# Optimization experiments

Measured on AMD Instinct MI355X. Metric: run time of the kernel, lower is better.

The kernel has to match this reference:

```python
import jax, jax.numpy as jnp
import numpy as np

NHEAD = 8
HEAD_DIM = 32  # per-head dim d; C = NHEAD * HEAD_DIM = 256
NEG_INF = -1e9


def setup_inputs() -> dict:
    key = jax.random.key(0)
    k1, k2, k3, k4, k5 = jax.random.split(key, 5)
    B, L, C = 8, 1024, NHEAD * HEAD_DIM
    query = jax.random.normal(k1, (B, L, C), dtype=jnp.float32)
    key_t = jax.random.normal(k2, (B, L, C), dtype=jnp.float32)
    value = jax.random.normal(k3, (B, L, C), dtype=jnp.float32)
    hard_mask = jax.random.randint(k4, (B, L), 0, 2).astype(bool)
    bias = jax.random.normal(k5, (B, L, L), dtype=jnp.float32)
    return {"query": query, "key": key_t, "value": value,
            "hard_mask": hard_mask, "bias": bias}


def reference(query, key, value, hard_mask, bias):
    # Faithful to the hard-mask path: attention is computed only among
    # active tokens (hard_mask True); inactive positions pass `value` through.
    # Masking inactive KEYS with -inf in the softmax is mathematically
    # identical to the sort/gather/slice/SDPA/scatter-unsort in the original.
    B, L, C = query.shape
    H, D = NHEAD, HEAD_DIM
    scale = 1.0 / jnp.sqrt(jnp.asarray(D, query.dtype))

    def split_heads(t):  # (B, L, C) -> (B, H, L, D)
        return t.reshape(B, L, H, D).transpose(0, 2, 1, 3)

    q, k, v = split_heads(query), split_heads(key), split_heads(value)

    # scores: (B, H, Lq, Lk); bias broadcasts over heads
    scores = jnp.einsum('bhld,bhmd->bhlm', q, k) * scale + bias[:, None, :, :]
    scores = jnp.where(hard_mask[:, None, None, :], scores, NEG_INF)
    attn = jax.nn.softmax(scores, axis=-1)
    out = jnp.einsum('bhlm,bhmd->bhld', attn, v)          # (B, H, L, D)
    out = out.transpose(0, 2, 1, 3).reshape(B, L, C)      # (B, L, C)

    # inactive query positions return the raw value (scatter-back behavior)
    out = jnp.where(hard_mask[:, :, None], out, value)

    # torch.stack over per-item (1, L, C) results -> (B, 1, L, C)
    return out[:, None, :, :]
```

## Files before the change

kernel.cpp:

```cpp
#include <hip/hip_runtime.h>
#include <hip/hip_bf16.h>

#define B_    8
#define H_    8
#define L_    1024
#define D_    32
#define C_    256
#define NK    64
#define PSTR  72

typedef __attribute__((ext_vector_type(8))) short bf16x8;
typedef __attribute__((ext_vector_type(4))) float f32x4;

__device__ inline unsigned short f2bf(float f) {
    union { float f; unsigned int u; } x; x.f = f;
    return (unsigned short)((x.u + 0x7fffu + ((x.u >> 16) & 1u)) >> 16);
}

__device__ inline unsigned int pk_bf16(float lo, float hi) {
    union { __hip_bfloat162 h; unsigned int u; } c;
    c.h = __float22bfloat162_rn(make_float2(lo, hi));
    return c.u;
}

__global__ __launch_bounds__(256) void prep_all(
    const float* __restrict__ k, const float* __restrict__ v,
    const float* __restrict__ bias, const int* __restrict__ mask,
    unsigned short* __restrict__ kfrag, unsigned short* __restrict__ vfrag,
    unsigned short* __restrict__ bfragT)
{
    const int tid = threadIdx.x;
    const int blk = blockIdx.x;
    __shared__ float sKf[64 * 36];
    __shared__ float sVf[64 * 33];
    __shared__ float sMadd[L_];

    if (blk < 1024) {
        const int bh = blk >> 4, c = blk & 15;
        const int b = bh >> 3, h = bh & 7;
        {
            const int row = tid >> 2, seg = tid & 3;
            const size_t src = (size_t)(b * L_ + c * 64 + row) * C_ + h * D_ + seg * 8;
            float4 a = *(const float4*)(k + src);
            float4 d = *(const float4*)(k + src + 4);
            *(float4*)(sKf + row * 36 + seg * 8) = a;
            *(float4*)(sKf + row * 36 + seg * 8 + 4) = d;
            float4 va = *(const float4*)(v + src);
            float4 vd = *(const float4*)(v + src + 4);
            float* vr = sVf + row * 33 + seg * 8;
            vr[0] = va.x; vr[1] = va.y; vr[2] = va.z; vr[3] = va.w;
            vr[4] = vd.x; vr[5] = vd.y; vr[6] = vd.z; vr[7] = vd.w;
        }
        __syncthreads();
        const int ln = tid & 63, u = tid >> 6;
        const int l16 = ln & 15, quad = ln >> 4;
        {
            const float* src = sKf + (u * 16 + l16) * 36 + quad * 8;
            float4 a = *(const float4*)src;
            float4 d = *(const float4*)(src + 4);
            uint4 o = { pk_bf16(a.x, a.y), pk_bf16(a.z, a.w),
                        pk_bf16(d.x, d.y), pk_bf16(d.z, d.w) };
            *(uint4*)(kfrag + (size_t)blk * 2048 + u * 512 + ln * 8) = o;
        }
        {
            const int s2 = u >> 1, nt = u & 1;
            float vals[8];
#pragma unroll
            for (int j = 0; j < 8; ++j)
                vals[j] = sVf[(s2 * 32 + quad * 8 + j) * 33 + nt * 16 + l16];
            uint4 o = { pk_bf16(vals[0], vals[1]), pk_bf16(vals[2], vals[3]),
                        pk_bf16(vals[4], vals[5]), pk_bf16(vals[6], vals[7]) };
            *(uint4*)(vfrag + (size_t)blk * 2048 + s2 * 1024 + nt * 512 + ln * 8) = o;
        }
    } else {
        const int bblk = blk - 1024;
        const int b = bblk >> 6, strip = bblk & 63;
        {
            int4 m = ((const int4*)(mask + b * L_))[tid];
            sMadd[tid * 4 + 0] = m.x ? 0.f : -1e9f;
            sMadd[tid * 4 + 1] = m.y ? 0.f : -1e9f;
            sMadd[tid * 4 + 2] = m.z ? 0.f : -1e9f;
            sMadd[tid * 4 + 3] = m.w ? 0.f : -1e9f;
        }
        __syncthreads();
        const int l16 = tid >> 4, ntp = (tid >> 2) & 3, qp = tid & 3;
        const float* brow = bias + ((size_t)(b * L_) + strip * 16 + l16) * L_;
        unsigned short* obase = bfragT + (size_t)bblk * 16384
                                + (qp * 16 + l16) * 16 + ntp * 4;
        const int koff = ntp * 16 + qp * 4;
#pragma unroll 4
        for (int c = 0; c < 16; ++c) {
            const int key = c * 64 + koff;
            float4 a = *(const float4*)(brow + key);
            const float* mp = sMadd + key;
            uint2 o = { pk_bf16(a.x + mp[0], a.y + mp[1]),
                        pk_bf16(a.z + mp[2], a.w + mp[3]) };
            *(uint2*)(obase + c * 1024) = o;
        }
    }
}

__global__ __launch_bounds__(256, 4) void attn_fa3(
    const float* __restrict__ q,
    const float* __restrict__ v,
    const int*   __restrict__ mask,
    const unsigned short* __restrict__ kfrag,
    const unsigned short* __restrict__ vfrag,
    const unsigned short* __restrict__ bfragT,
    float*       __restrict__ out)
{
    __shared__ __align__(16) unsigned short sP[4][16 * PSTR];

    const int tid  = threadIdx.x;
    const int wv   = tid >> 6;
    const int ln   = tid & 63;
    const int l16  = ln & 15;
    const int quad = ln >> 4;

    const int blk = blockIdx.x;
    const int h   = blk >> 7;
    const int rem = blk & 127;
    const int b   = rem >> 4;
    const int qt  = rem & 15;
    const int strip = qt * 4 + wv;
    const int q0  = strip * 16;
    const int bh  = b * H_ + h;

    const float scale = 0.17677669529663687f;

    bf16x8 qfrag;
    {
        const float* qp = q + ((size_t)(b * L_ + q0 + l16) * C_ + h * D_ + quad * 8);
        float4 a = ((const float4*)qp)[0];
        float4 c = ((const float4*)qp)[1];
        __align__(16) unsigned int u[4] = {
            pk_bf16(a.x * scale, a.y * scale), pk_bf16(a.z * scale, a.w * scale),
            pk_bf16(c.x * scale, c.y * scale), pk_bf16(c.z * scale, c.w * scale)};
        qfrag = *(const bf16x8*)u;
    }

    bf16x8 onesf;
#pragma unroll
    for (int i = 0; i < 8; ++i) onesf[i] = (short)0x3F80;

    const unsigned short* kf_base = kfrag  + (size_t)bh * 32768 + ln * 8;
    const unsigned short* vf_base = vfrag  + (size_t)bh * 32768 + ln * 8;
    const unsigned short* bm_base = bfragT + (size_t)(b * 64 + strip) * 16384 + ln * 16;
    unsigned short* const sPw = &sP[wv][0];

    f32x4 Oacc[2] = {{0.f,0.f,0.f,0.f},{0.f,0.f,0.f,0.f}};
    f32x4 Lacc    = {0.f,0.f,0.f,0.f};

    bf16x8 kf[4];
    uint4  bm[2];
#pragma unroll
    for (int nt = 0; nt < 4; ++nt)
        kf[nt] = *(const bf16x8*)(kf_base + nt * 512);
    bm[0] = *(const uint4*)(bm_base);
    bm[1] = *(const uint4*)(bm_base + 8);

    for (int c = 0; c < 16; ++c) {
        bf16x8 vf[4];
#pragma unroll
        for (int u2 = 0; u2 < 4; ++u2)
            vf[u2] = *(const bf16x8*)(vf_base + c * 2048 + u2 * 512);

        f32x4 S[4];
#pragma unroll
        for (int nt = 0; nt < 4; ++nt)
            S[nt] = __builtin_amdgcn_mfma_f32_16x16x32_bf16(
                kf[nt], qfrag, (f32x4){0.f,0.f,0.f,0.f}, 0, 0, 0);

        const int cn = (c < 15) ? c + 1 : 15;
        bf16x8 kfN[4];
        uint4  bmN[2];
#pragma unroll
        for (int nt = 0; nt < 4; ++nt)
            kfN[nt] = *(const bf16x8*)(kf_base + cn * 2048 + nt * 512);
        bmN[0] = *(const uint4*)(bm_base + cn * 1024);
        bmN[1] = *(const uint4*)(bm_base + cn * 1024 + 8);

        unsigned short* const prow = sPw + l16 * PSTR + quad * 4;
#pragma unroll
        for (int nt = 0; nt < 4; ++nt) {
            const unsigned int w0 = ((const unsigned int*)bm)[2 * nt];
            const unsigned int w1 = ((const unsigned int*)bm)[2 * nt + 1];
            const float b0 = __uint_as_float(w0 << 16);
            const float b1 = __uint_as_float(w0 & 0xffff0000u);
            const float b2 = __uint_as_float(w1 << 16);
            const float b3 = __uint_as_float(w1 & 0xffff0000u);
            const float p0 = __expf(S[nt][0] + b0);
            const float p1 = __expf(S[nt][1] + b1);
            const float p2 = __expf(S[nt][2] + b2);
            const float p3 = __expf(S[nt][3] + b3);
            uint2 pw = { pk_bf16(p0, p1), pk_bf16(p2, p3) };
            *(uint2*)(prow + nt * 16) = pw;
        }

#pragma unroll
        for (int s2 = 0; s2 < 2; ++s2) {
            bf16x8 pf = *(const bf16x8*)(sPw + l16 * PSTR + s2 * 32 + quad * 8);
            Lacc = __builtin_amdgcn_mfma_f32_16x16x32_bf16(pf, onesf, Lacc, 0, 0, 0);
            Oacc[0] = __builtin_amdgcn_mfma_f32_16x16x32_bf16(pf, vf[s2 * 2 + 0], Oacc[0], 0, 0, 0);
            Oacc[1] = __builtin_amdgcn_mfma_f32_16x16x32_bf16(pf, vf[s2 * 2 + 1], Oacc[1], 0, 0, 0);
        }

#pragma unroll
        for (int nt = 0; nt < 4; ++nt) kf[nt] = kfN[nt];
        bm[0] = bmN[0];
        bm[1] = bmN[1];
    }

#pragma unroll
    for (int r = 0; r < 4; ++r) {
        const int qrow = q0 + quad * 4 + r;
        const int active = mask[b * L_ + qrow];
        const float inv = 1.f / Lacc[r];
        const size_t base = (size_t)(b * L_ + qrow) * C_ + h * D_;
#pragma unroll
        for (int nt = 0; nt < 2; ++nt) {
            const size_t idx = base + nt * 16 + l16;
            out[idx] = active ? Oacc[nt][r] * inv : v[idx];
        }
    }
}

#define MQ    64
#define KSTR  48
#define VSTR  72

__global__ __launch_bounds__(256) void masked_attn_mfma(
    const float* __restrict__ q,
    const float* __restrict__ k,
    const float* __restrict__ v,
    const int*   __restrict__ mask,
    const float* __restrict__ bias,
    float*       __restrict__ out)
{
    __shared__ __align__(16) unsigned short sQ[MQ][KSTR];
    __shared__ __align__(16) unsigned short sKt[NK][KSTR];
    __shared__ __align__(16) unsigned short sVt[D_][VSTR];
    __shared__ __align__(16) unsigned short sP2[4][16][VSTR];
    __shared__ float sMadd2[NK];

    const int tid  = threadIdx.x;
    const int wv   = tid >> 6;
    const int ln   = tid & 63;
    const int l16  = ln & 15;
    const int quad = ln >> 4;

    const int blk = blockIdx.x;
    const int h   = blk & 7;
    const int qt  = (blk >> 3) & 15;
    const int b   = blk >> 7;
    const int q0  = qt * MQ;
    const float scale = 0.17677669529663687f;

    {
        const int row = tid >> 2, d0 = (tid & 3) * 8;
        const float* src = q + ((size_t)(b * L_ + q0 + row) * C_ + h * D_ + d0);
        float4 a = ((const float4*)src)[0];
        float4 c = ((const float4*)src)[1];
        __align__(16) unsigned short t8[8] = {
            f2bf(a.x), f2bf(a.y), f2bf(a.z), f2bf(a.w),
            f2bf(c.x), f2bf(c.y), f2bf(c.z), f2bf(c.w)};
        *(int4*)&sQ[row][d0] = *(const int4*)t8;
    }
    __syncthreads();

    const bf16x8 qfrag = *(const bf16x8*)&sQ[wv * 16 + l16][quad * 8];
    f32x4 Oacc[2] = {{0.f,0.f,0.f,0.f},{0.f,0.f,0.f,0.f}};
    float lsum[4] = {0.f, 0.f, 0.f, 0.f};

    for (int j0 = 0; j0 < L_; j0 += NK) {
        __syncthreads();
        {
            const int row = tid >> 2, d0 = (tid & 3) * 8;
            const size_t src = (size_t)(b * L_ + j0 + row) * C_ + h * D_ + d0;
            float4 ka = ((const float4*)(k + src))[0];
            float4 kb = ((const float4*)(k + src))[1];
            __align__(16) unsigned short t8[8] = {
                f2bf(ka.x), f2bf(ka.y), f2bf(ka.z), f2bf(ka.w),
                f2bf(kb.x), f2bf(kb.y), f2bf(kb.z), f2bf(kb.w)};
            *(int4*)&sKt[row][d0] = *(const int4*)t8;

            float4 va = ((const float4*)(v + src))[0];
            float4 vb = ((const float4*)(v + src))[1];
            sVt[d0 + 0][row] = f2bf(va.x);
            sVt[d0 + 1][row] = f2bf(va.y);
            sVt[d0 + 2][row] = f2bf(va.z);
            sVt[d0 + 3][row] = f2bf(va.w);
            sVt[d0 + 4][row] = f2bf(vb.x);
            sVt[d0 + 5][row] = f2bf(vb.y);
            sVt[d0 + 6][row] = f2bf(vb.z);
            sVt[d0 + 7][row] = f2bf(vb.w);
            if (tid < NK) sMadd2[tid] = mask[b * L_ + j0 + tid] ? 0.f : -1e9f;
        }
        __syncthreads();

        bf16x8 kf[4];
#pragma unroll
        for (int nt = 0; nt < 4; ++nt)
            kf[nt] = *(const bf16x8*)&sKt[nt * 16 + l16][quad * 8];

        f32x4 S[4];
#pragma unroll
        for (int nt = 0; nt < 4; ++nt)
            S[nt] = __builtin_amdgcn_mfma_f32_16x16x32_bf16(
                qfrag, kf[nt], (f32x4){0.f,0.f,0.f,0.f}, 0, 0, 0);

        float psum[4] = {0.f, 0.f, 0.f, 0.f};
        const size_t brow0 = (size_t)(b * L_ + q0 + wv * 16 + quad * 4) * L_ + j0;
#pragma unroll
        for (int nt = 0; nt < 4; ++nt) {
            const float madd = sMadd2[nt * 16 + l16];
#pragma unroll
            for (int r = 0; r < 4; ++r) {
                float s = S[nt][r] * scale + bias[brow0 + (size_t)r * L_ + nt * 16 + l16] + madd;
                float p = __expf(s);
                psum[r] += p;
                S[nt][r] = p;
            }
        }
#pragma unroll
        for (int nt = 0; nt < 4; ++nt)
#pragma unroll
            for (int r = 0; r < 4; ++r)
                sP2[wv][quad * 4 + r][nt * 16 + l16] = f2bf(S[nt][r]);
#pragma unroll
        for (int r = 0; r < 4; ++r) {
            float t = psum[r];
            t += __shfl_xor(t, 1);
            t += __shfl_xor(t, 2);
            t += __shfl_xor(t, 4);
            t += __shfl_xor(t, 8);
            lsum[r] += t;
        }
#pragma unroll
        for (int s2 = 0; s2 < 2; ++s2) {
            bf16x8 pf = *(const bf16x8*)&sP2[wv][l16][s2 * 32 + quad * 8];
#pragma unroll
            for (int nt = 0; nt < 2; ++nt) {
                bf16x8 vf = *(const bf16x8*)&sVt[nt * 16 + l16][s2 * 32 + quad * 8];
                Oacc[nt] = __builtin_amdgcn_mfma_f32_16x16x32_bf16(pf, vf, Oacc[nt], 0, 0, 0);
            }
        }
    }
#pragma unroll
    for (int r = 0; r < 4; ++r) {
        const int qg = q0 + wv * 16 + quad * 4 + r;
        const int active = mask[b * L_ + qg];
        const size_t obase = (size_t)(b * L_ + qg) * C_ + h * D_;
        const float inv = 1.f / lsum[r];
#pragma unroll
        for (int nt = 0; nt < 2; ++nt) {
            float val;
            if (active) val = Oacc[nt][r] * inv;
            else        val = v[obase + nt * 16 + l16];
            out[obase + nt * 16 + l16] = val;
        }
    }
}

extern "C" void kernel_launch(void* const* d_in, const int* in_sizes, int n_in,
                              void* d_out, int out_size, void* d_ws, size_t ws_size,
                              hipStream_t stream) {
    const float* q    = (const float*)d_in[0];
    const float* k    = (const float*)d_in[1];
    const float* v    = (const float*)d_in[2];
    const int*   mask = (const int*)d_in[3];
    const float* bias = (const float*)d_in[4];
    float* out = (float*)d_out;

    if (ws_size >= (size_t)24 * 1024 * 1024) {
        unsigned short* kfrag  = (unsigned short*)d_ws;
        unsigned short* vfrag  = kfrag + (size_t)2 * 1024 * 1024;
        unsigned short* bfragT = vfrag + (size_t)2 * 1024 * 1024;
        prep_all<<<1536, 256, 0, stream>>>(k, v, bias, mask, kfrag, vfrag, bfragT);
        attn_fa3<<<1024, 256, 0, stream>>>(q, v, mask, kfrag, vfrag, bfragT, out);
    } else {
        masked_attn_mfma<<<1024, 256, 0, stream>>>(q, k, v, mask, bias, out);
    }
}
```

Measured before the change: 130.5 us.

## Process two query strips per wave to reuse K/V fragments

```diff
diff --git a/kernel.cpp b/kernel.cpp
--- a/kernel.cpp
+++ b/kernel.cpp
@@ -100,7 +100,7 @@
     }
 }
 
-__global__ __launch_bounds__(256, 4) void attn_fa3(
+__global__ __launch_bounds__(128, 2) void attn_fa5(
     const float* __restrict__ q,
     const float* __restrict__ v,
     const int*   __restrict__ mask,
@@ -109,7 +109,7 @@
     const unsigned short* __restrict__ bfragT,
     float*       __restrict__ out)
 {
-    __shared__ __align__(16) unsigned short sP[4][16 * PSTR];
+    __shared__ __align__(16) unsigned short sP[2][32 * PSTR];
 
     const int tid  = threadIdx.x;
     const int wv   = tid >> 6;
@@ -122,21 +122,22 @@
     const int rem = blk & 127;
     const int b   = rem >> 4;
     const int qt  = rem & 15;
-    const int strip = qt * 4 + wv;
-    const int q0  = strip * 16;
+    const int q0  = qt * 64 + wv * 32;
+    const int strip0 = q0 >> 4;
     const int bh  = b * H_ + h;
 
     const float scale = 0.17677669529663687f;
 
-    bf16x8 qfrag;
-    {
-        const float* qp = q + ((size_t)(b * L_ + q0 + l16) * C_ + h * D_ + quad * 8);
+    bf16x8 qfrag[2];
+#pragma unroll
+    for (int st = 0; st < 2; ++st) {
+        const float* qp = q + ((size_t)(b * L_ + q0 + st * 16 + l16) * C_ + h * D_ + quad * 8);
         float4 a = ((const float4*)qp)[0];
         float4 c = ((const float4*)qp)[1];
         __align__(16) unsigned int u[4] = {
             pk_bf16(a.x * scale, a.y * scale), pk_bf16(a.z * scale, a.w * scale),
             pk_bf16(c.x * scale, c.y * scale), pk_bf16(c.z * scale, c.w * scale)};
-        qfrag = *(const bf16x8*)u;
+        qfrag[st] = *(const bf16x8*)u;
     }
 
     bf16x8 onesf;
@@ -145,19 +146,25 @@
 
     const unsigned short* kf_base = kfrag  + (size_t)bh * 32768 + ln * 8;
     const unsigned short* vf_base = vfrag  + (size_t)bh * 32768 + ln * 8;
-    const unsigned short* bm_base = bfragT + (size_t)(b * 64 + strip) * 16384 + ln * 16;
+    const unsigned short* bm_base[2] = {
+        bfragT + (size_t)(b * 64 + strip0    ) * 16384 + ln * 16,
+        bfragT + (size_t)(b * 64 + strip0 + 1) * 16384 + ln * 16 };
     unsigned short* const sPw = &sP[wv][0];
 
-    f32x4 Oacc[2] = {{0.f,0.f,0.f,0.f},{0.f,0.f,0.f,0.f}};
-    f32x4 Lacc    = {0.f,0.f,0.f,0.f};
+    f32x4 Oacc[2][2] = {{{0.f,0.f,0.f,0.f},{0.f,0.f,0.f,0.f}},
+                        {{0.f,0.f,0.f,0.f},{0.f,0.f,0.f,0.f}}};
+    f32x4 Lacc[2]    = {{0.f,0.f,0.f,0.f},{0.f,0.f,0.f,0.f}};
 
     bf16x8 kf[4];
-    uint4  bm[2];
+    uint4  bm[2][2];
 #pragma unroll
     for (int nt = 0; nt < 4; ++nt)
         kf[nt] = *(const bf16x8*)(kf_base + nt * 512);
-    bm[0] = *(const uint4*)(bm_base);
-    bm[1] = *(const uint4*)(bm_base + 8);
+#pragma unroll
+    for (int st = 0; st < 2; ++st) {
+        bm[st][0] = *(const uint4*)(bm_base[st]);
+        bm[st][1] = *(const uint4*)(bm_base[st] + 8);
+    }
 
     for (int c = 0; c < 16; ++c) {
         bf16x8 vf[4];
@@ -165,62 +172,80 @@
         for (int u2 = 0; u2 < 4; ++u2)
             vf[u2] = *(const bf16x8*)(vf_base + c * 2048 + u2 * 512);
 
-        f32x4 S[4];
-#pragma unroll
-        for (int nt = 0; nt < 4; ++nt)
-            S[nt] = __builtin_amdgcn_mfma_f32_16x16x32_bf16(
-                kf[nt], qfrag, (f32x4){0.f,0.f,0.f,0.f}, 0, 0, 0);
+        f32x4 S[2][4];
+#pragma unroll
+        for (int st = 0; st < 2; ++st)
+#pragma unroll
+            for (int nt = 0; nt < 4; ++nt)
+                S[st][nt] = __builtin_amdgcn_mfma_f32_16x16x32_bf16(
+                    kf[nt], qfrag[st], (f32x4){0.f,0.f,0.f,0.f}, 0, 0, 0);
 
         const int cn = (c < 15) ? c + 1 : 15;
         bf16x8 kfN[4];
-        uint4  bmN[2];
+        uint4  bmN[2][2];
 #pragma unroll
         for (int nt = 0; nt < 4; ++nt)
             kfN[nt] = *(const bf16x8*)(kf_base + cn * 2048 + nt * 512);
-        bmN[0] = *(const uint4*)(bm_base + cn * 1024);
-        bmN[1] = *(const uint4*)(bm_base + cn * 1024 + 8);
-
-        unsigned short* const prow = sPw + l16 * PSTR + quad * 4;
-#pragma unroll
-        for (int nt = 0; nt < 4; ++nt) {
-            const unsigned int w0 = ((const unsigned int*)bm)[2 * nt];
-            const unsigned int w1 = ((const unsigned int*)bm)[2 * nt + 1];
-            const float b0 = __uint_as_float(w0 << 16);
-            const float b1 = __uint_as_float(w0 & 0xffff0000u);
-            const float b2 = __uint_as_float(w1 << 16);
-            const float b3 = __uint_as_float(w1 & 0xffff0000u);
-            const float p0 = __expf(S[nt][0] + b0);
-            const float p1 = __expf(S[nt][1] + b1);
-            const float p2 = __expf(S[nt][2] + b2);
-            const float p3 = __expf(S[nt][3] + b3);
-            uint2 pw = { pk_bf16(p0, p1), pk_bf16(p2, p3) };
-            *(uint2*)(prow + nt * 16) = pw;
-        }
-
-#pragma unroll
-        for (int s2 = 0; s2 < 2; ++s2) {
-            bf16x8 pf = *(const bf16x8*)(sPw + l16 * PSTR + s2 * 32 + quad * 8);
-            Lacc = __builtin_amdgcn_mfma_f32_16x16x32_bf16(pf, onesf, Lacc, 0, 0, 0);
-            Oacc[0] = __builtin_amdgcn_mfma_f32_16x16x32_bf16(pf, vf[s2 * 2 + 0], Oacc[0], 0, 0, 0);
-            Oacc[1] = __builtin_amdgcn_mfma_f32_16x16x32_bf16(pf, vf[s2 * 2 + 1], Oacc[1], 0, 0, 0);
+#pragma unroll
+        for (int st = 0; st < 2; ++st) {
+            bmN[st][0] = *(const uint4*)(bm_base[st] + cn * 1024);
+            bmN[st][1] = *(const uint4*)(bm_base[st] + cn * 1024 + 8);
+        }
+
+#pragma unroll
+        for (int st = 0; st < 2; ++st) {
+            unsigned short* const prow = sPw + (st * 16 + l16) * PSTR + quad * 4;
+            const unsigned int* bw = (const unsigned int*)&bm[st][0];
+#pragma unroll
+            for (int nt = 0; nt < 4; ++nt) {
+                const unsigned int w0 = bw[2 * nt];
+                const unsigned int w1 = bw[2 * nt + 1];
+                const float b0 = __uint_as_float(w0 << 16);
+                const float b1 = __uint_as_float(w0 & 0xffff0000u);
+                const float b2 = __uint_as_float(w1 << 16);
+                const float b3 = __uint_as_float(w1 & 0xffff0000u);
+                const float p0 = __expf(S[st][nt][0] + b0);
+                const float p1 = __expf(S[st][nt][1] + b1);
+                const float p2 = __expf(S[st][nt][2] + b2);
+                const float p3 = __expf(S[st][nt][3] + b3);
+                uint2 pw = { pk_bf16(p0, p1), pk_bf16(p2, p3) };
+                *(uint2*)(prow + nt * 16) = pw;
+            }
+        }
+
+#pragma unroll
+        for (int st = 0; st < 2; ++st) {
+#pragma unroll
+            for (int s2 = 0; s2 < 2; ++s2) {
+                bf16x8 pf = *(const bf16x8*)(sPw + (st * 16 + l16) * PSTR + s2 * 32 + quad * 8);
+                Lacc[st] = __builtin_amdgcn_mfma_f32_16x16x32_bf16(pf, onesf, Lacc[st], 0, 0, 0);
+                Oacc[st][0] = __builtin_amdgcn_mfma_f32_16x16x32_bf16(pf, vf[s2 * 2 + 0], Oacc[st][0], 0, 0, 0);
+                Oacc[st][1] = __builtin_amdgcn_mfma_f32_16x16x32_bf16(pf, vf[s2 * 2 + 1], Oacc[st][1], 0, 0, 0);
+            }
         }
 
 #pragma unroll
         for (int nt = 0; nt < 4; ++nt) kf[nt] = kfN[nt];
-        bm[0] = bmN[0];
-        bm[1] = bmN[1];
-    }
-
-#pragma unroll
-    for (int r = 0; r < 4; ++r) {
-        const int qrow = q0 + quad * 4 + r;
-        const int active = mask[b * L_ + qrow];
-        const float inv = 1.f / Lacc[r];
-        const size_t base = (size_t)(b * L_ + qrow) * C_ + h * D_;
-#pragma unroll
-        for (int nt = 0; nt < 2; ++nt) {
-            const size_t idx = base + nt * 16 + l16;
-            out[idx] = active ? Oacc[nt][r] * inv : v[idx];
+#pragma unroll
+        for (int st = 0; st < 2; ++st) {
+            bm[st][0] = bmN[st][0];
+            bm[st][1] = bmN[st][1];
+        }
+    }
+
+#pragma unroll
+    for (int st = 0; st < 2; ++st) {
+#pragma unroll
+        for (int r = 0; r < 4; ++r) {
+            const int qrow = q0 + st * 16 + quad * 4 + r;
+            const int active = mask[b * L_ + qrow];
+            const float inv = 1.f / Lacc[st][r];
+            const size_t base = (size_t)(b * L_ + qrow) * C_ + h * D_;
+#pragma unroll
+            for (int nt = 0; nt < 2; ++nt) {
+                const size_t idx = base + nt * 16 + l16;
+                out[idx] = active ? Oacc[st][nt][r] * inv : v[idx];
+            }
         }
     }
 }
@@ -377,7 +402,7 @@
         unsigned short* vfrag  = kfrag + (size_t)2 * 1024 * 1024;
         unsigned short* bfragT = vfrag + (size_t)2 * 1024 * 1024;
         prep_all<<<1536, 256, 0, stream>>>(k, v, bias, mask, kfrag, vfrag, bfragT);
-        attn_fa3<<<1024, 256, 0, stream>>>(q, v, mask, kfrag, vfrag, bfragT, out);
+        attn_fa5<<<1024, 128, 0, stream>>>(q, v, mask, kfrag, vfrag, bfragT, out);
     } else {
         masked_attn_mfma<<<1024, 256, 0, stream>>>(q, k, v, mask, bias, out);
     }
```

Result: no change. 130.2 us (-0.2%).
